# Optimization experiments

Measured on AMD Instinct MI355X. Metric: run time of the kernel, lower is better.

Reference implementation:

```python
import jax, jax.numpy as jnp
import numpy as np

N = 100000      # nodes
E = 1600000     # edges
G = 2000        # molecules (graphs)
F = 40          # node features
FE = 16         # edge features
H = 64          # conv width
HM = 128        # mlp width
C = 2           # classes
NEG_SLOPE = 0.01
BN_EPS = 1e-5


def leaky(x):
    return jnp.where(x >= 0, x, NEG_SLOPE * x)


def batch_norm(x, g, b):
    # training-mode BatchNorm over the node axis (biased variance, eps=1e-5)
    m = jnp.mean(x, axis=0)
    v = jnp.var(x, axis=0)
    return (x - m) * jax.lax.rsqrt(v + BN_EPS) * g + b


def setup_inputs() -> dict:
    key = jax.random.key(0)
    ks = iter(jax.random.split(key, 100))

    def nrm(shape, s=1.0):
        return jax.random.normal(next(ks), shape, dtype=jnp.float32) * s

    inp = {}
    inp["x"] = nrm((N, F))
    inp["edge_index"] = jax.random.randint(next(ks), (2, E), 0, N, dtype=jnp.int32)
    inp["edge_attr"] = nrm((E, FE))
    inp["batch"] = jnp.repeat(jnp.arange(G, dtype=jnp.int32), N // G)

    dims = [(F, H), (H, H), (H, H)]
    for i, (ci, co) in enumerate(dims):
        inp[f"conv{i}_eps"] = jnp.zeros((1,), dtype=jnp.float32)
        inp[f"conv{i}_We"] = nrm((FE, ci), 1.0 / np.sqrt(FE))
        inp[f"conv{i}_be"] = nrm((ci,), 0.05)
        inp[f"conv{i}_W1"] = nrm((ci, co), 1.0 / np.sqrt(ci))
        inp[f"conv{i}_b1"] = nrm((co,), 0.05)
        inp[f"conv{i}_g1"] = 1.0 + nrm((co,), 0.05)
        inp[f"conv{i}_bt1"] = nrm((co,), 0.05)
        inp[f"conv{i}_W2"] = nrm((co, co), 1.0 / np.sqrt(co))
        inp[f"conv{i}_b2"] = nrm((co,), 0.05)
        inp[f"bn{i}_g"] = 1.0 + nrm((co,), 0.05)
        inp[f"bn{i}_b"] = nrm((co,), 0.05)

    inp["mlp0_W"] = nrm((2 * H, HM), 1.0 / np.sqrt(2 * H))
    inp["mlp0_b"] = nrm((HM,), 0.05)
    inp["mlp1_W"] = nrm((HM, HM), 1.0 / np.sqrt(HM))
    inp["mlp1_b"] = nrm((HM,), 0.05)
    inp["final_W"] = nrm((HM, C), 1.0 / np.sqrt(HM))
    inp["final_b"] = nrm((C,), 0.05)
    return inp


def _forward(x, edge_attr, edge_index, batch, convs, mlps, final_W, final_b):
    src, dst = edge_index[0], edge_index[1]
    for (eps, We, be, W1, b1, g1, bt1, W2, b2, bg, bb) in convs:
        # GINEConv: msg = relu(x_src + lin_edge(edge_attr)); scatter-add to dst
        e = edge_attr @ We + be                    # [E, in]
        msg = jax.nn.relu(x[src] + e)              # gather + fuse
        agg = jax.ops.segment_sum(msg, dst, num_segments=x.shape[0])
        h = (1.0 + eps) * x + agg
        # conv nn: Linear -> BatchNorm -> LeakyReLU -> Linear
        h = batch_norm(h @ W1 + b1, g1, bt1)
        h = leaky(h) @ W2 + b2
        # outer BatchNorm + LeakyReLU
        x = leaky(batch_norm(h, bg, bb))
    # global_add_pool then repeat_interleave by per-mol counts == pool[batch]
    pool = jax.ops.segment_sum(x, batch, num_segments=G)
    x = jnp.concatenate([x, pool[batch]], axis=1)  # [N, 2H]
    for (W, b) in mlps:
        x = leaky(x @ W + b)  # dropout is identity in eval mode
    return x @ final_W + final_b


def reference(x, edge_index, edge_attr, batch,
              conv0_eps, conv0_We, conv0_be, conv0_W1, conv0_b1, conv0_g1, conv0_bt1, conv0_W2, conv0_b2, bn0_g, bn0_b,
              conv1_eps, conv1_We, conv1_be, conv1_W1, conv1_b1, conv1_g1, conv1_bt1, conv1_W2, conv1_b2, bn1_g, bn1_b,
              conv2_eps, conv2_We, conv2_be, conv2_W1, conv2_b1, conv2_g1, conv2_bt1, conv2_W2, conv2_b2, bn2_g, bn2_b,
              mlp0_W, mlp0_b, mlp1_W, mlp1_b, final_W, final_b):
    convs = [
        (conv0_eps, conv0_We, conv0_be, conv0_W1, conv0_b1, conv0_g1, conv0_bt1, conv0_W2, conv0_b2, bn0_g, bn0_b),
        (conv1_eps, conv1_We, conv1_be, conv1_W1, conv1_b1, conv1_g1, conv1_bt1, conv1_W2, conv1_b2, bn1_g, bn1_b),
        (conv2_eps, conv2_We, conv2_be, conv2_W1, conv2_b1, conv2_g1, conv2_bt1, conv2_W2, conv2_b2, bn2_g, bn2_b),
    ]
    mlps = [(mlp0_W, mlp0_b), (mlp1_W, mlp1_b)]
    return _forward(x, edge_attr, edge_index, batch, convs, mlps, final_W, final_b)
```

## Files before the change

### kernel.cpp

```cpp
#include <hip/hip_runtime.h>


#define N_  100000
#define E_  1600000
#define G_  2000
#define SCAN_NB 196
#define NBLK 1563

typedef _Float16 half2v __attribute__((ext_vector_type(2)));

__device__ __forceinline__ float leaky_(float z) { return z >= 0.f ? z : 0.01f * z; }

__device__ __forceinline__ half2v u2h(unsigned u) {
    union { unsigned u; half2v h; } c; c.u = u; return c.h;
}

__device__ __forceinline__ float dot2_(half2v a, half2v b, float c) {
#if __has_builtin(__builtin_amdgcn_fdot2)
    return __builtin_amdgcn_fdot2(a, b, c, false);
#else
    return c + (float)a.x * (float)b.x + (float)a.y * (float)b.y;
#endif
}

__global__ __launch_bounds__(256) void hist_rank_kernel(
    const int* __restrict__ dst, int* __restrict__ cnt, int* __restrict__ rank)
{
#pragma unroll 4
    for (int e = blockIdx.x * 256 + threadIdx.x; e < E_; e += gridDim.x * 256)
        rank[e] = atomicAdd(&cnt[dst[e]], 1);
}

__global__ __launch_bounds__(256) void scanA(
    const int* __restrict__ cnt, int* __restrict__ blocksum)
{
    __shared__ int s[256];
    const int t = threadIdx.x, b = blockIdx.x;
    const int i0 = (b * 256 + t) * 2;
    int v = 0;
    if (i0 < N_) v += cnt[i0];
    if (i0 + 1 < N_) v += cnt[i0 + 1];
    s[t] = v; __syncthreads();
    for (int o = 128; o > 0; o >>= 1) { if (t < o) s[t] += s[t + o]; __syncthreads(); }
    if (t == 0) blocksum[b] = s[0];
}

__global__ __launch_bounds__(256) void scanB(
    const int* __restrict__ blocksum, int* __restrict__ blockpref)
{
    __shared__ int s[256];
    const int t = threadIdx.x;
    int v = (t < SCAN_NB) ? blocksum[t] : 0;
    s[t] = v; __syncthreads();
    for (int o = 1; o < 256; o <<= 1) {
        int u = (t >= o) ? s[t - o] : 0;
        __syncthreads(); s[t] += u; __syncthreads();
    }
    blockpref[t] = s[t] - v;
}

__global__ __launch_bounds__(256) void scanC(
    const int* __restrict__ cnt, int* __restrict__ off,
    const int* __restrict__ blockpref)
{
    __shared__ int s[256];
    const int t = threadIdx.x, b = blockIdx.x;
    const int i0 = (b * 256 + t) * 2;
    int v0 = (i0 < N_) ? cnt[i0] : 0;
    int v1 = (i0 + 1 < N_) ? cnt[i0 + 1] : 0;
    int pv = v0 + v1;
    s[t] = pv; __syncthreads();
    for (int o = 1; o < 256; o <<= 1) {
        int u = (t >= o) ? s[t - o] : 0;
        __syncthreads(); s[t] += u; __syncthreads();
    }
    int run = blockpref[b] + s[t] - pv;
    if (i0 < N_) {
        off[i0] = run; run += v0;
        if (i0 + 1 < N_) off[i0 + 1] = run;
    }
    if (b == 0 && t == 0) off[N_] = E_;
}

__global__ __launch_bounds__(256) void place_kernel(
    const int* __restrict__ src, const int* __restrict__ dst,
    const int* __restrict__ rank, const int* __restrict__ off,
    int2* __restrict__ se)
{
#pragma unroll 4
    for (int e = blockIdx.x * 256 + threadIdx.x; e < E_; e += gridDim.x * 256) {
        const int p = off[dst[e]] + rank[e];
        se[p] = make_int2(src[e], e);
    }
}

#define DPW 13
#define CHUNK 32

template<int CI, int APPLY_BN>
__global__ __launch_bounds__(256, 4) void agg_sorted(
    const float* __restrict__ edge_attr,
    const int2* __restrict__ se,
    const int* __restrict__ off,
    const float* __restrict__ We, const float* __restrict__ be,
    const float* __restrict__ x,
    const float* __restrict__ stIn,
    const float* __restrict__ bng, const float* __restrict__ bnb,
    float* __restrict__ agg)
{
    __shared__ __align__(16) unsigned s_ea[4][2][CHUNK * 8];
    __shared__ int s_src[4][2][CHUNK];
    const int t = threadIdx.x;
    const int lane = t & 63;
    const int w = t >> 6;
    const int wid = __builtin_amdgcn_readfirstlane(blockIdx.x * 4 + w);

    half2v wh[8];
#pragma unroll
    for (int k = 0; k < 8; ++k) wh[k] = half2v{(_Float16)0.f, (_Float16)0.f};
    float beL = 0.f, scL = 1.f, shL = 0.f;
    if (lane < CI) {
#pragma unroll
        for (int k = 0; k < 8; ++k)
            wh[k] = half2v{(_Float16)We[(2 * k) * CI + lane],
                           (_Float16)We[(2 * k + 1) * CI + lane]};
        beL = be[lane];
        if (APPLY_BN) {
            float mean = stIn[lane] * (1.0f / N_);
            float var  = stIn[64 + lane] * (1.0f / N_) - mean * mean;
            scL = bng[lane] * rsqrtf(var + 1e-5f);
            shL = bnb[lane] - mean * scL;
        }
    }
    const int ln = (lane < CI) ? lane : 0;

    const int d0 = wid * DPW;
    if (d0 >= N_) return;
    const int d1 = min(d0 + DPW, N_);
    const int pw0 = off[d0];
    const int pw1 = off[d1];
    if (pw0 >= pw1) {
        for (int d = d0; d < d1; ++d)
            if (lane < CI) agg[(size_t)d * CI + lane] = 0.f;
        return;
    }

    int d = d0;
    int e1 = off[d0 + 1];
    float acc = 0.f;
    int buf = 0;
    const int r = lane >> 1;
    const int hf = lane & 1;

    {
        const int m0 = min(CHUNK, pw1 - pw0);
        int2 t0 = make_int2(0, 0);
        if (lane < m0) t0 = se[pw0 + lane];
        int e = __shfl(t0.y, r);
        if (r >= m0) e = 0;
        const float4* ep = (const float4*)(edge_attr + (size_t)e * 16 + hf * 8);
        float4 f0 = ep[0], f1 = ep[1];
        union { uint4 u; half2v h[4]; } cv;
        cv.h[0] = half2v{(_Float16)f0.x, (_Float16)f0.y};
        cv.h[1] = half2v{(_Float16)f0.z, (_Float16)f0.w};
        cv.h[2] = half2v{(_Float16)f1.x, (_Float16)f1.y};
        cv.h[3] = half2v{(_Float16)f1.z, (_Float16)f1.w};
        *(uint4*)&s_ea[w][0][r * 8 + hf * 4] = cv.u;
        if (lane < CHUNK) s_src[w][0][lane] = (lane < m0) ? t0.x : 0;
    }
    int2 pse = make_int2(0, 0);
    {
        const int np = pw0 + CHUNK;
        const int nm = min(CHUNK, pw1 - np);
        if (nm > 0 && lane < nm) pse = se[np + lane];
    }
    __builtin_amdgcn_wave_barrier();

    for (int cp = pw0; cp < pw1; cp += CHUNK) {
        const int m = min(CHUNK, pw1 - cp);
        const int np = cp + CHUNK;
        const int nm = min(CHUNK, pw1 - np);
        const int np2 = cp + 2 * CHUNK;
        const int nm2 = min(CHUNK, pw1 - np2);

        float4 g0 = make_float4(0.f, 0.f, 0.f, 0.f), g1 = g0;
        if (nm > 0) {
            int ge = __shfl(pse.y, r);
            if (r >= nm) ge = 0;
            const float4* ep = (const float4*)(edge_attr + (size_t)ge * 16 + hf * 8);
            g0 = ep[0]; g1 = ep[1];
        }
        int2 nse = make_int2(0, 0);
        if (nm2 > 0 && lane < nm2) nse = se[np2 + lane];

        float xr[CHUNK];
#pragma unroll
        for (int i = 0; i < CHUNK; ++i) {
            const int s = s_src[w][buf][i];
            float raw = x[(size_t)s * CI + ln];
            xr[i] = APPLY_BN ? leaky_(raw * scL + shL) : raw;
        }
#pragma unroll
        for (int i = 0; i < CHUNK; ++i) {
            if (i >= m) break;
            while (cp + i == e1) {
                if (lane < CI) agg[(size_t)d * CI + lane] = acc;
                acc = 0.f; ++d;
                e1 = off[d + 1];
            }
            const unsigned* er = &s_ea[w][buf][i * 8];
            uint4 e0 = *(const uint4*)&er[0];
            uint4 e2 = *(const uint4*)&er[4];
            float dotv = beL;
            dotv = dot2_(u2h(e0.x), wh[0], dotv);
            dotv = dot2_(u2h(e0.y), wh[1], dotv);
            dotv = dot2_(u2h(e0.z), wh[2], dotv);
            dotv = dot2_(u2h(e0.w), wh[3], dotv);
            dotv = dot2_(u2h(e2.x), wh[4], dotv);
            dotv = dot2_(u2h(e2.y), wh[5], dotv);
            dotv = dot2_(u2h(e2.z), wh[6], dotv);
            dotv = dot2_(u2h(e2.w), wh[7], dotv);
            float mm = xr[i] + dotv;
            acc += (mm > 0.f ? mm : 0.f);
        }

        if (nm > 0) {
            union { uint4 u; half2v h[4]; } cv;
            cv.h[0] = half2v{(_Float16)g0.x, (_Float16)g0.y};
            cv.h[1] = half2v{(_Float16)g0.z, (_Float16)g0.w};
            cv.h[2] = half2v{(_Float16)g1.x, (_Float16)g1.y};
            cv.h[3] = half2v{(_Float16)g1.z, (_Float16)g1.w};
            *(uint4*)&s_ea[w][buf ^ 1][r * 8 + hf * 4] = cv.u;
            if (lane < CHUNK) s_src[w][buf ^ 1][lane] = (lane < nm) ? pse.x : 0;
        }
        pse = nse;
        __builtin_amdgcn_wave_barrier();
        buf ^= 1;
    }

    while (d < d1) {
        if (lane < CI) agg[(size_t)d * CI + lane] = acc;
        acc = 0.f; ++d;
    }
}

template<int CI, int MODE, int BNIN>
__global__ __launch_bounds__(256, 4) void node_gemm(
    const float* __restrict__ in,
    const float* __restrict__ agg,
    const float* __restrict__ eps,
    const float* __restrict__ g1,
    const float* __restrict__ bt1,
    const float* __restrict__ stIn,
    const float* __restrict__ W, const float* __restrict__ bias_,
    float* __restrict__ outbuf, float* __restrict__ partial)
{
    __shared__ __align__(16) float a_lds[64][CI + 4];
    __shared__ __align__(16) float w_lds[CI][68];
    __shared__ float s_sc[64], s_sh[64];
    const int t = threadIdx.x;
    const int n0 = blockIdx.x * 64;
    constexpr int QR = CI / 4;

    if (MODE == 1 || BNIN) {
        if (t < 64) {
            float mean = stIn[t] * (1.0f / N_);
            float var  = stIn[64 + t] * (1.0f / N_) - mean * mean;
            float sc = g1[t] * rsqrtf(var + 1e-5f);
            s_sc[t] = sc;
            s_sh[t] = bt1[t] - mean * sc;
        }
        __syncthreads();
    }

    if (MODE == 0) {
        const float hs = 1.0f + eps[0];
        for (int f = t; f < 64 * QR; f += 256) {
            int i = f / QR, q = f - i * QR;
            int n = n0 + i;
            float4 val = make_float4(0.f, 0.f, 0.f, 0.f);
            if (n < N_) {
                float4 xa = *(const float4*)&in[(size_t)n * CI + q * 4];
                float4 ag = *(const float4*)&agg[(size_t)n * CI + q * 4];
                if (BNIN) {
                    int c = q * 4;
                    xa.x = leaky_(xa.x * s_sc[c]     + s_sh[c]);
                    xa.y = leaky_(xa.y * s_sc[c + 1] + s_sh[c + 1]);
                    xa.z = leaky_(xa.z * s_sc[c + 2] + s_sh[c + 2]);
                    xa.w = leaky_(xa.w * s_sc[c + 3] + s_sh[c + 3]);
                }
                val = make_float4(hs * xa.x + ag.x, hs * xa.y + ag.y,
                                  hs * xa.z + ag.z, hs * xa.w + ag.w);
            }
            *(float4*)&a_lds[i][q * 4] = val;
        }
    } else {
        for (int f = t; f < 64 * QR; f += 256) {
            int i = f / QR, q = f - i * QR;
            int n = n0 + i;
            float4 val = make_float4(0.f, 0.f, 0.f, 0.f);
            if (n < N_) {
                float4 uv = *(const float4*)&in[(size_t)n * CI + q * 4];
                int c = q * 4;
                val = make_float4(leaky_(uv.x * s_sc[c]     + s_sh[c]),
                                  leaky_(uv.y * s_sc[c + 1] + s_sh[c + 1]),
                                  leaky_(uv.z * s_sc[c + 2] + s_sh[c + 2]),
                                  leaky_(uv.w * s_sc[c + 3] + s_sh[c + 3]));
            }
            *(float4*)&a_lds[i][q * 4] = val;
        }
    }
    for (int f = t; f < CI * 16; f += 256) {
        int k = f >> 4, cq = f & 15;
        *(float4*)&w_lds[k][cq * 4] = *(const float4*)&W[k * 64 + cq * 4];
    }
    __syncthreads();

    const int tr = t & 15;
    const int c0 = (t >> 4) * 4;
    float acc[4][4] = {};
#pragma unroll 2
    for (int k = 0; k < CI; k += 4) {
        float ar[4][4];
#pragma unroll
        for (int j = 0; j < 4; ++j)
            *(float4*)&ar[j][0] = *(const float4*)&a_lds[tr + 16 * j][k];
#pragma unroll
        for (int kk = 0; kk < 4; ++kk) {
            float4 b = *(const float4*)&w_lds[k + kk][c0];
#pragma unroll
            for (int j = 0; j < 4; ++j) {
                acc[j][0] += ar[j][kk] * b.x;
                acc[j][1] += ar[j][kk] * b.y;
                acc[j][2] += ar[j][kk] * b.z;
                acc[j][3] += ar[j][kk] * b.w;
            }
        }
    }

    const float4 bb = *(const float4*)&bias_[c0];
    const float bias[4] = { bb.x, bb.y, bb.z, bb.w };
    float ls[4] = {}, lq[4] = {};
#pragma unroll
    for (int j = 0; j < 4; ++j) {
        int n = n0 + tr + 16 * j;
        if (n < N_) {
            float o[4];
#pragma unroll
            for (int cc = 0; cc < 4; ++cc) {
                o[cc] = acc[j][cc] + bias[cc];
                ls[cc] += o[cc];
                lq[cc] += o[cc] * o[cc];
            }
            *(float4*)&outbuf[(size_t)n * 64 + c0] = make_float4(o[0], o[1], o[2], o[3]);
        }
    }
#pragma unroll
    for (int m = 1; m <= 8; m <<= 1) {
#pragma unroll
        for (int cc = 0; cc < 4; ++cc) {
            ls[cc] += __shfl_xor(ls[cc], m);
            lq[cc] += __shfl_xor(lq[cc], m);
        }
    }
    if (tr == 0) {
#pragma unroll
        for (int cc = 0; cc < 4; ++cc) {
            partial[(size_t)(c0 + cc) * NBLK + blockIdx.x]      = ls[cc];
            partial[(size_t)(64 + c0 + cc) * NBLK + blockIdx.x] = lq[cc];
        }
    }
}

__global__ __launch_bounds__(256) void finalize_stats(
    const float* __restrict__ partial, float* __restrict__ stats)
{
    const int c = blockIdx.x;
    const int t = threadIdx.x;
    float s = 0.f;
    for (int b = t; b < NBLK; b += 256) s += partial[(size_t)c * NBLK + b];
    __shared__ float red[256];
    red[t] = s; __syncthreads();
    for (int o = 128; o > 0; o >>= 1) { if (t < o) red[t] += red[t + o]; __syncthreads(); }
    if (t == 0) stats[c] = red[0];
}

__global__ __launch_bounds__(256) void pool_kernel(
    const float* __restrict__ v, const float* __restrict__ st,
    const float* __restrict__ bg, const float* __restrict__ bb,
    float* __restrict__ pool)
{
    const int c = threadIdx.x & 63;
    const int g = blockIdx.x * 4 + (threadIdx.x >> 6);
    float mean = st[c] * (1.0f / N_);
    float var  = st[64 + c] * (1.0f / N_) - mean * mean;
    float sc = bg[c] * rsqrtf(var + 1e-5f);
    float sh = bb[c] - mean * sc;
    const float* p = v + (size_t)g * 50 * 64 + c;
    float s = 0.f;
#pragma unroll
    for (int j = 0; j < 50; ++j) s += leaky_(p[(size_t)j * 64] * sc + sh);
    pool[(size_t)g * 64 + c] = s;
}

__global__ __launch_bounds__(256) void pool_mlp0(
    const float* __restrict__ pool, const float* __restrict__ W0,
    const float* __restrict__ b0, float* __restrict__ g0)
{
    const int t = threadIdx.x;
    const int g = blockIdx.x * 2 + (t >> 7);
    const int c = t & 127;
    float s = b0[c];
    const float* pr = pool + (size_t)g * 64;
#pragma unroll 4
    for (int k = 0; k < 64; ++k)
        s += pr[k] * W0[(size_t)(64 + k) * 128 + c];
    g0[(size_t)g * 128 + c] = s;
}

__global__ __launch_bounds__(256, 2) void mlp_kernel(
    const float* __restrict__ v, const float* __restrict__ st,
    const float* __restrict__ bg, const float* __restrict__ bb,
    const float* __restrict__ g0,
    const float* __restrict__ W0,
    const float* __restrict__ W1, const float* __restrict__ b1,
    const float* __restrict__ Wf, const float* __restrict__ bf,
    float* __restrict__ out)
{
    __shared__ __align__(16) float a_lds[128][132];
    __shared__ __align__(16) float w_lds[16][132];
    __shared__ __align__(16) float sWfT[2][128];
    __shared__ float s_scm[64], s_shm[64];
    __shared__ int sbid[128];
    const int t = threadIdx.x;
    const int n0 = blockIdx.x * 128;

    if (t < 64) {
        float mean = st[t] * (1.0f / N_);
        float var  = st[64 + t] * (1.0f / N_) - mean * mean;
        float sc = bg[t] * rsqrtf(var + 1e-5f);
        s_scm[t] = sc;
        s_shm[t] = bb[t] - mean * sc;
    }
    __syncthreads();

    for (int f = t; f < 128 * 16; f += 256) {
        int i = f >> 4, q = f & 15;
        int n = n0 + i;
        float4 val = make_float4(0.f, 0.f, 0.f, 0.f);
        if (n < N_) {
            float4 xv = *(const float4*)&v[(size_t)n * 64 + q * 4];
            int c = q * 4;
            val = make_float4(leaky_(xv.x * s_scm[c]     + s_shm[c]),
                              leaky_(xv.y * s_scm[c + 1] + s_shm[c + 1]),
                              leaky_(xv.z * s_scm[c + 2] + s_shm[c + 2]),
                              leaky_(xv.w * s_scm[c + 3] + s_shm[c + 3]));
        }
        *(float4*)&a_lds[i][q * 4] = val;
    }
    if (t < 128) {
        int n = n0 + t;
        sbid[t] = (n < N_) ? (n / 50) : (G_ - 1);
        sWfT[0][t] = Wf[t * 2];
        sWfT[1][t] = Wf[t * 2 + 1];
    }

    const int tr = t & 15;
    const int c0 = (t >> 4) * 8;
    float acc[8][8];

#pragma unroll
    for (int j = 0; j < 8; ++j)
#pragma unroll
        for (int cc = 0; cc < 8; ++cc) acc[j][cc] = 0.f;

    for (int kc = 0; kc < 64; kc += 16) {
        __syncthreads();
        for (int f = t; f < 16 * 32; f += 256) {
            int k = f >> 5, cq = f & 31;
            *(float4*)&w_lds[k][cq * 4] = *(const float4*)&W0[(size_t)(kc + k) * 128 + cq * 4];
        }
        __syncthreads();
        for (int k = 0; k < 16; k += 4) {
            float ar[8][4];
#pragma unroll
            for (int j = 0; j < 8; ++j)
                *(float4*)&ar[j][0] = *(const float4*)&a_lds[tr + 16 * j][kc + k];
#pragma unroll
            for (int kk = 0; kk < 4; ++kk) {
                float4 bA = *(const float4*)&w_lds[k + kk][c0];
                float4 bB = *(const float4*)&w_lds[k + kk][c0 + 4];
#pragma unroll
                for (int j = 0; j < 8; ++j) {
                    acc[j][0] += ar[j][kk] * bA.x;
                    acc[j][1] += ar[j][kk] * bA.y;
                    acc[j][2] += ar[j][kk] * bA.z;
                    acc[j][3] += ar[j][kk] * bA.w;
                    acc[j][4] += ar[j][kk] * bB.x;
                    acc[j][5] += ar[j][kk] * bB.y;
                    acc[j][6] += ar[j][kk] * bB.z;
                    acc[j][7] += ar[j][kk] * bB.w;
                }
            }
        }
    }
    __syncthreads();
#pragma unroll
    for (int j = 0; j < 8; ++j) {
        int row = tr + 16 * j;
        const float* gr = g0 + (size_t)sbid[row] * 128;
        float4 gA = *(const float4*)&gr[c0];
        float4 gB = *(const float4*)&gr[c0 + 4];
        float o[8] = { acc[j][0] + gA.x, acc[j][1] + gA.y, acc[j][2] + gA.z, acc[j][3] + gA.w,
                       acc[j][4] + gB.x, acc[j][5] + gB.y, acc[j][6] + gB.z, acc[j][7] + gB.w };
#pragma unroll
        for (int cc = 0; cc < 8; ++cc) o[cc] = leaky_(o[cc]);
        *(float4*)&a_lds[row][c0]     = make_float4(o[0], o[1], o[2], o[3]);
        *(float4*)&a_lds[row][c0 + 4] = make_float4(o[4], o[5], o[6], o[7]);
    }

#pragma unroll
    for (int j = 0; j < 8; ++j)
#pragma unroll
        for (int cc = 0; cc < 8; ++cc) acc[j][cc] = 0.f;

    for (int kc = 0; kc < 128; kc += 16) {
        __syncthreads();
        for (int f = t; f < 16 * 32; f += 256) {
            int k = f >> 5, cq = f & 31;
            *(float4*)&w_lds[k][cq * 4] = *(const float4*)&W1[(size_t)(kc + k) * 128 + cq * 4];
        }
        __syncthreads();
        for (int k = 0; k < 16; k += 4) {
            float ar[8][4];
#pragma unroll
            for (int j = 0; j < 8; ++j)
                *(float4*)&ar[j][0] = *(const float4*)&a_lds[tr + 16 * j][kc + k];
#pragma unroll
            for (int kk = 0; kk < 4; ++kk) {
                float4 bA = *(const float4*)&w_lds[k + kk][c0];
                float4 bB = *(const float4*)&w_lds[k + kk][c0 + 4];
#pragma unroll
                for (int j = 0; j < 8; ++j) {
                    acc[j][0] += ar[j][kk] * bA.x;
                    acc[j][1] += ar[j][kk] * bA.y;
                    acc[j][2] += ar[j][kk] * bA.z;
                    acc[j][3] += ar[j][kk] * bA.w;
                    acc[j][4] += ar[j][kk] * bB.x;
                    acc[j][5] += ar[j][kk] * bB.y;
                    acc[j][6] += ar[j][kk] * bB.z;
                    acc[j][7] += ar[j][kk] * bB.w;
                }
            }
        }
    }
    __syncthreads();
    {
        float4 bb0 = *(const float4*)&b1[c0];
        float4 bb1 = *(const float4*)&b1[c0 + 4];
        float bias[8] = { bb0.x, bb0.y, bb0.z, bb0.w, bb1.x, bb1.y, bb1.z, bb1.w };
#pragma unroll
        for (int j = 0; j < 8; ++j) {
            int row = tr + 16 * j;
            float o[8];
#pragma unroll
            for (int cc = 0; cc < 8; ++cc) o[cc] = leaky_(acc[j][cc] + bias[cc]);
            *(float4*)&a_lds[row][c0]     = make_float4(o[0], o[1], o[2], o[3]);
            *(float4*)&a_lds[row][c0 + 4] = make_float4(o[4], o[5], o[6], o[7]);
        }
    }
    __syncthreads();

    {
        int i = t >> 1, c = t & 1;
        int n = n0 + i;
        if (n < N_) {
            float s = bf[c];
            for (int k = 0; k < 128; k += 4) {
                float4 av = *(const float4*)&a_lds[i][k];
                float4 wv = *(const float4*)&sWfT[c][k];
                s += av.x * wv.x + av.y * wv.y + av.z * wv.z + av.w * wv.w;
            }
            out[(size_t)n * 2 + c] = s;
        }
    }
}

extern "C" void kernel_launch(void* const* d_in, const int* in_sizes, int n_in,
                              void* d_out, int out_size, void* d_ws, size_t ws_size,
                              hipStream_t stream)
{
    (void)in_sizes; (void)n_in; (void)out_size; (void)ws_size;

    const float* x0    = (const float*)d_in[0];
    const int*   eidx  = (const int*)d_in[1];
    const float* eattr = (const float*)d_in[2];
    const float* L[3][11];
    for (int l = 0; l < 3; ++l)
        for (int j = 0; j < 11; ++j)
            L[l][j] = (const float*)d_in[4 + l * 11 + j];
    const float* mlp0W = (const float*)d_in[37];
    const float* mlp0b = (const float*)d_in[38];
    const float* mlp1W = (const float*)d_in[39];
    const float* mlp1b = (const float*)d_in[40];
    const float* finW  = (const float*)d_in[41];
    const float* finb  = (const float*)d_in[42];
    float* out = (float*)d_out;

    float* ws    = (float*)d_ws;
    float* P0    = ws;
    float* P1    = P0 + (size_t)N_ * 64;
    float* P2    = P1 + (size_t)N_ * 64;
    float* pool  = P2 + (size_t)N_ * 64;
    float* g0    = pool + (size_t)G_ * 64;
    float* stats = g0   + (size_t)G_ * 128;
    float* partial = stats + 768;
    int*   off   = (int*)(partial + 128 * NBLK);
    int*   cnt   = off + (N_ + 2);
    int*   bsum  = cnt + N_;
    int*   bpref = bsum + 256;
    int*   rank  = bpref + 256;
    int2*  se    = (int2*)(rank + E_);

    const int* src = eidx;
    const int* dst = eidx + E_;
    const int GB = NBLK;

    hipMemsetAsync(cnt, 0, (size_t)N_ * sizeof(int), stream);
    hist_rank_kernel<<<2048, 256, 0, stream>>>(dst, cnt, rank);
    scanA<<<SCAN_NB, 256, 0, stream>>>(cnt, bsum);
    scanB<<<1, 256, 0, stream>>>(bsum, bpref);
    scanC<<<SCAN_NB, 256, 0, stream>>>(cnt, off, bpref);
    place_kernel<<<2048, 256, 0, stream>>>(src, dst, rank, off, se);

    const int AGGB = ((N_ + DPW - 1) / DPW + 3) / 4 + 1;

    for (int l = 0; l < 3; ++l) {
        float* s1 = stats + (2 * l) * 128;
        float* s2 = stats + (2 * l + 1) * 128;
        if (l == 0) {
            agg_sorted<40, 0><<<AGGB, 256, 0, stream>>>(eattr, se, off, L[0][1], L[0][2],
                                                        x0, nullptr, nullptr, nullptr, P0);
            node_gemm<40, 0, 0><<<GB, 256, 0, stream>>>(x0, P0, L[0][0], nullptr, nullptr, nullptr,
                                                        L[0][3], L[0][4], P1, partial);
        } else {
            float* sp = stats + (2 * l - 1) * 128;
            agg_sorted<64, 1><<<AGGB, 256, 0, stream>>>(eattr, se, off, L[l][1], L[l][2],
                                                        P2, sp, L[l - 1][9], L[l - 1][10], P0);
            node_gemm<64, 0, 1><<<GB, 256, 0, stream>>>(P2, P0, L[l][0], L[l - 1][9], L[l - 1][10], sp,
                                                        L[l][3], L[l][4], P1, partial);
        }
        finalize_stats<<<128, 256, 0, stream>>>(partial, s1);
        node_gemm<64, 1, 0><<<GB, 256, 0, stream>>>(P1, nullptr, nullptr, L[l][5], L[l][6], s1,
                                                    L[l][7], L[l][8], P2, partial);
        finalize_stats<<<128, 256, 0, stream>>>(partial, s2);
    }

    float* sF = stats + 5 * 128;
    pool_kernel<<<G_ / 4, 256, 0, stream>>>(P2, sF, L[2][9], L[2][10], pool);
    pool_mlp0<<<G_ / 2, 256, 0, stream>>>(pool, mlp0W, mlp0b, g0);
    mlp_kernel<<<(N_ + 127) / 128, 256, 0, stream>>>(P2, sF, L[2][9], L[2][10], g0, mlp0W,
                                                     mlp1W, mlp1b, finW, finb, out);
}
```

Measured before the change: 892.2 us.

## Pre-convert edge attributes to fp16 once and double node GEMM row tile

Adds a kernel that converts edge_attr to fp16 once per call. The three aggregation passes then gather half-size rows (32 bytes instead of 64 per edge) with no per-pass conversion. Separately, node_gemm now handles 128 rows per block instead of 64, with each thread accumulating 8 rows, and launch bounds drop to 3 blocks per CU. This halves the block and partial-sum counts but raises register and LDS pressure, and the extra conversion pass adds one full read and write of edge_attr.

```diff
diff --git a/kernel.cpp b/kernel.cpp
--- a/kernel.cpp
+++ b/kernel.cpp
@@ -5,7 +5,7 @@
 #define E_  1600000
 #define G_  2000
 #define SCAN_NB 196
-#define NBLK 1563
+#define GB2 782
 
 typedef _Float16 half2v __attribute__((ext_vector_type(2)));
 
@@ -94,12 +94,24 @@
     }
 }
 
+__global__ __launch_bounds__(256) void eacvt_kernel(
+    const float* __restrict__ edge_attr, unsigned short* __restrict__ ea16)
+{
+    for (int i = blockIdx.x * 256 + threadIdx.x; i < E_ * 4; i += gridDim.x * 256) {
+        float4 f = ((const float4*)edge_attr)[i];
+        union { unsigned long long u; half2v h[2]; } cv;
+        cv.h[0] = half2v{(_Float16)f.x, (_Float16)f.y};
+        cv.h[1] = half2v{(_Float16)f.z, (_Float16)f.w};
+        ((unsigned long long*)ea16)[i] = cv.u;
+    }
+}
+
 #define DPW 13
 #define CHUNK 32
 
 template<int CI, int APPLY_BN>
 __global__ __launch_bounds__(256, 4) void agg_sorted(
-    const float* __restrict__ edge_attr,
+    const unsigned short* __restrict__ ea16,
     const int2* __restrict__ se,
     const int* __restrict__ off,
     const float* __restrict__ We, const float* __restrict__ be,
@@ -158,14 +170,8 @@
         if (lane < m0) t0 = se[pw0 + lane];
         int e = __shfl(t0.y, r);
         if (r >= m0) e = 0;
-        const float4* ep = (const float4*)(edge_attr + (size_t)e * 16 + hf * 8);
-        float4 f0 = ep[0], f1 = ep[1];
-        union { uint4 u; half2v h[4]; } cv;
-        cv.h[0] = half2v{(_Float16)f0.x, (_Float16)f0.y};
-        cv.h[1] = half2v{(_Float16)f0.z, (_Float16)f0.w};
-        cv.h[2] = half2v{(_Float16)f1.x, (_Float16)f1.y};
-        cv.h[3] = half2v{(_Float16)f1.z, (_Float16)f1.w};
-        *(uint4*)&s_ea[w][0][r * 8 + hf * 4] = cv.u;
+        uint4 v = ((const uint4*)(ea16 + (size_t)e * 16))[hf];
+        *(uint4*)&s_ea[w][0][r * 8 + hf * 4] = v;
         if (lane < CHUNK) s_src[w][0][lane] = (lane < m0) ? t0.x : 0;
     }
     int2 pse = make_int2(0, 0);
@@ -183,12 +189,11 @@
         const int np2 = cp + 2 * CHUNK;
         const int nm2 = min(CHUNK, pw1 - np2);
 
-        float4 g0 = make_float4(0.f, 0.f, 0.f, 0.f), g1 = g0;
+        uint4 g = make_uint4(0, 0, 0, 0);
         if (nm > 0) {
             int ge = __shfl(pse.y, r);
             if (r >= nm) ge = 0;
-            const float4* ep = (const float4*)(edge_attr + (size_t)ge * 16 + hf * 8);
-            g0 = ep[0]; g1 = ep[1];
+            g = ((const uint4*)(ea16 + (size_t)ge * 16))[hf];
         }
         int2 nse = make_int2(0, 0);
         if (nm2 > 0 && lane < nm2) nse = se[np2 + lane];
@@ -225,12 +230,7 @@
         }
 
         if (nm > 0) {
-            union { uint4 u; half2v h[4]; } cv;
-            cv.h[0] = half2v{(_Float16)g0.x, (_Float16)g0.y};
-            cv.h[1] = half2v{(_Float16)g0.z, (_Float16)g0.w};
-            cv.h[2] = half2v{(_Float16)g1.x, (_Float16)g1.y};
-            cv.h[3] = half2v{(_Float16)g1.z, (_Float16)g1.w};
-            *(uint4*)&s_ea[w][buf ^ 1][r * 8 + hf * 4] = cv.u;
+            *(uint4*)&s_ea[w][buf ^ 1][r * 8 + hf * 4] = g;
             if (lane < CHUNK) s_src[w][buf ^ 1][lane] = (lane < nm) ? pse.x : 0;
         }
         pse = nse;
@@ -245,7 +245,7 @@
 }
 
 template<int CI, int MODE, int BNIN>
-__global__ __launch_bounds__(256, 4) void node_gemm(
+__global__ __launch_bounds__(256, 3) void node_gemm(
     const float* __restrict__ in,
     const float* __restrict__ agg,
     const float* __restrict__ eps,
@@ -255,11 +255,11 @@
     const float* __restrict__ W, const float* __restrict__ bias_,
     float* __restrict__ outbuf, float* __restrict__ partial)
 {
-    __shared__ __align__(16) float a_lds[64][CI + 4];
+    __shared__ __align__(16) float a_lds[128][CI + 4];
     __shared__ __align__(16) float w_lds[CI][68];
     __shared__ float s_sc[64], s_sh[64];
     const int t = threadIdx.x;
-    const int n0 = blockIdx.x * 64;
+    const int n0 = blockIdx.x * 128;
     constexpr int QR = CI / 4;
 
     if (MODE == 1 || BNIN) {
@@ -275,7 +275,7 @@
 
     if (MODE == 0) {
         const float hs = 1.0f + eps[0];
-        for (int f = t; f < 64 * QR; f += 256) {
+        for (int f = t; f < 128 * QR; f += 256) {
             int i = f / QR, q = f - i * QR;
             int n = n0 + i;
             float4 val = make_float4(0.f, 0.f, 0.f, 0.f);
@@ -295,7 +295,7 @@
             *(float4*)&a_lds[i][q * 4] = val;
         }
     } else {
-        for (int f = t; f < 64 * QR; f += 256) {
+        for (int f = t; f < 128 * QR; f += 256) {
             int i = f / QR, q = f - i * QR;
             int n = n0 + i;
             float4 val = make_float4(0.f, 0.f, 0.f, 0.f);
@@ -318,18 +318,18 @@
 
     const int tr = t & 15;
     const int c0 = (t >> 4) * 4;
-    float acc[4][4] = {};
+    float acc[8][4] = {};
 #pragma unroll 2
     for (int k = 0; k < CI; k += 4) {
-        float ar[4][4];
-#pragma unroll
-        for (int j = 0; j < 4; ++j)
+        float ar[8][4];
+#pragma unroll
+        for (int j = 0; j < 8; ++j)
             *(float4*)&ar[j][0] = *(const float4*)&a_lds[tr + 16 * j][k];
 #pragma unroll
         for (int kk = 0; kk < 4; ++kk) {
             float4 b = *(const float4*)&w_lds[k + kk][c0];
 #pragma unroll
-            for (int j = 0; j < 4; ++j) {
+            for (int j = 0; j < 8; ++j) {
                 acc[j][0] += ar[j][kk] * b.x;
                 acc[j][1] += ar[j][kk] * b.y;
                 acc[j][2] += ar[j][kk] * b.z;
@@ -342,7 +342,7 @@
     const float bias[4] = { bb.x, bb.y, bb.z, bb.w };
     float ls[4] = {}, lq[4] = {};
 #pragma unroll
-    for (int j = 0; j < 4; ++j) {
+    for (int j = 0; j < 8; ++j) {
         int n = n0 + tr + 16 * j;
         if (n < N_) {
             float o[4];
@@ -366,8 +366,8 @@
     if (tr == 0) {
 #pragma unroll
         for (int cc = 0; cc < 4; ++cc) {
-            partial[(size_t)(c0 + cc) * NBLK + blockIdx.x]      = ls[cc];
-            partial[(size_t)(64 + c0 + cc) * NBLK + blockIdx.x] = lq[cc];
+            partial[(size_t)(c0 + cc) * GB2 + blockIdx.x]      = ls[cc];
+            partial[(size_t)(64 + c0 + cc) * GB2 + blockIdx.x] = lq[cc];
         }
     }
 }
@@ -378,7 +378,7 @@
     const int c = blockIdx.x;
     const int t = threadIdx.x;
     float s = 0.f;
-    for (int b = t; b < NBLK; b += 256) s += partial[(size_t)c * NBLK + b];
+    for (int b = t; b < GB2; b += 256) s += partial[(size_t)c * GB2 + b];
     __shared__ float red[256];
     red[t] = s; __syncthreads();
     for (int o = 128; o > 0; o >>= 1) { if (t < o) red[t] += red[t + o]; __syncthreads(); }
@@ -615,19 +615,20 @@
     float* g0    = pool + (size_t)G_ * 64;
     float* stats = g0   + (size_t)G_ * 128;
     float* partial = stats + 768;
-    int*   off   = (int*)(partial + 128 * NBLK);
+    int*   off   = (int*)(partial + 128 * GB2);
     int*   cnt   = off + (N_ + 2);
     int*   bsum  = cnt + N_;
     int*   bpref = bsum + 256;
     int*   rank  = bpref + 256;
     int2*  se    = (int2*)(rank + E_);
+    unsigned short* ea16 = (unsigned short*)(se + E_);
 
     const int* src = eidx;
     const int* dst = eidx + E_;
-    const int GB = NBLK;
 
     hipMemsetAsync(cnt, 0, (size_t)N_ * sizeof(int), stream);
     hist_rank_kernel<<<2048, 256, 0, stream>>>(dst, cnt, rank);
+    eacvt_kernel<<<2048, 256, 0, stream>>>(eattr, ea16);
     scanA<<<SCAN_NB, 256, 0, stream>>>(cnt, bsum);
     scanB<<<1, 256, 0, stream>>>(bsum, bpref);
     scanC<<<SCAN_NB, 256, 0, stream>>>(cnt, off, bpref);
@@ -639,20 +640,20 @@
         float* s1 = stats + (2 * l) * 128;
         float* s2 = stats + (2 * l + 1) * 128;
         if (l == 0) {
-            agg_sorted<40, 0><<<AGGB, 256, 0, stream>>>(eattr, se, off, L[0][1], L[0][2],
+            agg_sorted<40, 0><<<AGGB, 256, 0, stream>>>(ea16, se, off, L[0][1], L[0][2],
                                                         x0, nullptr, nullptr, nullptr, P0);
-            node_gemm<40, 0, 0><<<GB, 256, 0, stream>>>(x0, P0, L[0][0], nullptr, nullptr, nullptr,
-                                                        L[0][3], L[0][4], P1, partial);
+            node_gemm<40, 0, 0><<<GB2, 256, 0, stream>>>(x0, P0, L[0][0], nullptr, nullptr, nullptr,
+                                                         L[0][3], L[0][4], P1, partial);
         } else {
             float* sp = stats + (2 * l - 1) * 128;
-            agg_sorted<64, 1><<<AGGB, 256, 0, stream>>>(eattr, se, off, L[l][1], L[l][2],
+            agg_sorted<64, 1><<<AGGB, 256, 0, stream>>>(ea16, se, off, L[l][1], L[l][2],
                                                         P2, sp, L[l - 1][9], L[l - 1][10], P0);
-            node_gemm<64, 0, 1><<<GB, 256, 0, stream>>>(P2, P0, L[l][0], L[l - 1][9], L[l - 1][10], sp,
-                                                        L[l][3], L[l][4], P1, partial);
+            node_gemm<64, 0, 1><<<GB2, 256, 0, stream>>>(P2, P0, L[l][0], L[l - 1][9], L[l - 1][10], sp,
+                                                         L[l][3], L[l][4], P1, partial);
         }
         finalize_stats<<<128, 256, 0, stream>>>(partial, s1);
-        node_gemm<64, 1, 0><<<GB, 256, 0, stream>>>(P1, nullptr, nullptr, L[l][5], L[l][6], s1,
-                                                    L[l][7], L[l][8], P2, partial);
+        node_gemm<64, 1, 0><<<GB2, 256, 0, stream>>>(P1, nullptr, nullptr, L[l][5], L[l][6], s1,
+                                                     L[l][7], L[l][8], P2, partial);
         finalize_stats<<<128, 256, 0, stream>>>(partial, s2);
     }
 
```

Result: slower. 945.5 us (+6.0%).
